# Performance work log

Measured on AMD Instinct MI355X. Metric: run time of the kernel, lower is better.

## Reference

```python
import jax, jax.numpy as jnp
import numpy as np

N_NODES = 50000
N_EDGES = 800000
IN_DIM = 128
OUT_DIM = 64
NEG_SLOPE = 0.01  # torch F.leaky_relu default


def setup_inputs() -> dict:
    key = jax.random.key(0)
    k1, k2, k3, k4, k5 = jax.random.split(key, 5)
    features = jax.random.normal(k1, (N_NODES, IN_DIM), dtype=jnp.float32)
    # xavier-ish scale for weights
    fc_w = jax.random.normal(k2, (OUT_DIM, IN_DIM), dtype=jnp.float32) * (1.0 / np.sqrt(IN_DIM))
    attn_w = jax.random.normal(k3, (2 * OUT_DIM,), dtype=jnp.float32) * (1.0 / np.sqrt(2 * OUT_DIM))
    src = jax.random.randint(k4, (N_EDGES,), 0, N_NODES, dtype=jnp.int32)
    dst = jax.random.randint(k5, (N_EDGES,), 0, N_NODES, dtype=jnp.int32)
    return {"features": features, "fc_w": fc_w, "attn_w": attn_w, "src": src, "dst": dst}


def reference(features, fc_w, attn_w, src, dst):
    n = features.shape[0]
    out_dim = fc_w.shape[0]
    # z = fc(features), [N, out_dim]
    z = features @ fc_w.T
    # attn_fc([z_src || z_dst]) = z_src @ w_src + z_dst @ w_dst
    a_src = z @ attn_w[:out_dim]   # [N]
    a_dst = z @ attn_w[out_dim:]   # [N]
    e = a_src[src] + a_dst[dst]    # [E] per-edge raw score
    e = jnp.where(e > 0, e, NEG_SLOPE * e)  # leaky_relu
    # edge softmax over incoming edges of each dst node
    e_max = jax.ops.segment_max(e, dst, num_segments=n)      # [N]
    w = jnp.exp(e - e_max[dst])                               # [E]
    denom = jax.ops.segment_sum(w, dst, num_segments=n)       # [N]
    # weighted neighbor sum: sum_e alpha_e * z[src_e]
    num = jax.ops.segment_sum(w[:, None] * z[src], dst, num_segments=n)  # [N, out_dim]
    h = num / jnp.where(denom > 0, denom, 1.0)[:, None]
    # activation = elu
    h = jax.nn.elu(h)
    return h
```

## Files before the change

kernel.cpp:

```cpp
#include <hip/hip_runtime.h>
#include <hip/hip_bf16.h>

#define N_NODES 50000
#define N_EDGES 800000
#define IN_DIM 128
#define OUT_DIM 64
#define NEG_SLOPE 0.01f
#define NEG_INF (-3.0e38f)

#define N_STRIPS (N_NODES / 16)
#define Z_BLOCKS ((N_STRIPS + 3) / 4)
#define E_I4 (N_EDGES / 4)

#define NB ((N_NODES + 127) / 128)
#define CAP_B 3072
#define CNT_STRIDE 16
#define EB 100
#define CHUNK_I4 (E_I4 / EB)

typedef __bf16 bf16x8 __attribute__((ext_vector_type(8)));
typedef float f32x4 __attribute__((ext_vector_type(4)));

__device__ __forceinline__ float rlanef(float v, int l) {
  return __uint_as_float(__builtin_amdgcn_readlane(__float_as_uint(v), l));
}
__device__ __forceinline__ int rlanei(int v, int l) {
  return __builtin_amdgcn_readlane(v, l);
}

__device__ __forceinline__ unsigned short f2bf_us(float f) {
  __hip_bfloat16 h = __float2bfloat16(f);
  return *reinterpret_cast<unsigned short*>(&h);
}
__device__ __forceinline__ bf16x8 pack_bf16(float4 lo, float4 hi) {
  union { bf16x8 v; unsigned short u[8]; } r;
  r.u[0] = f2bf_us(lo.x); r.u[1] = f2bf_us(lo.y);
  r.u[2] = f2bf_us(lo.z); r.u[3] = f2bf_us(lo.w);
  r.u[4] = f2bf_us(hi.x); r.u[5] = f2bf_us(hi.y);
  r.u[6] = f2bf_us(hi.z); r.u[7] = f2bf_us(hi.w);
  return r.v;
}

__global__ __launch_bounds__(256) void gat_z_bucket(
    const float* __restrict__ feat, const float* __restrict__ fcw,
    const float* __restrict__ attnw, __hip_bfloat16* __restrict__ z,
    float* __restrict__ asrc, float* __restrict__ adst,
    const int* __restrict__ src, const int* __restrict__ dst,
    int* __restrict__ cnt, unsigned* __restrict__ pairs) {
  if (blockIdx.x >= Z_BLOCKS) {
    __shared__ int hist[NB];
    __shared__ int curs[NB];
    const int tid = threadIdx.x;
    const int i0 = (blockIdx.x - Z_BLOCKS) * CHUNK_I4;
    for (int i = tid; i < NB; i += 256) hist[i] = 0;
    __syncthreads();
    for (int t = i0 + tid; t < i0 + CHUNK_I4; t += 256) {
      int4 d = ((const int4*)dst)[t];
      atomicAdd(&hist[d.x >> 7], 1);
      atomicAdd(&hist[d.y >> 7], 1);
      atomicAdd(&hist[d.z >> 7], 1);
      atomicAdd(&hist[d.w >> 7], 1);
    }
    __syncthreads();
    for (int i = tid; i < NB; i += 256) {
      int h = hist[i];
      curs[i] = h ? atomicAdd(cnt + i * CNT_STRIDE, h) : 0;
    }
    __syncthreads();
    for (int t = i0 + tid; t < i0 + CHUNK_I4; t += 256) {
      int4 s = ((const int4*)src)[t];
      int4 d = ((const int4*)dst)[t];
#define BKT_PUT(dd, ss)                                                    \
  {                                                                        \
    int b = (dd) >> 7;                                                     \
    int r = atomicAdd(&curs[b], 1);                                        \
    if (r < CAP_B)                                                         \
      pairs[(size_t)b * CAP_B + r] =                                       \
          ((unsigned)((dd) & 127) << 16) | (unsigned)(ss);                 \
  }
      BKT_PUT(d.x, s.x)
      BKT_PUT(d.y, s.y)
      BKT_PUT(d.z, s.z)
      BKT_PUT(d.w, s.w)
#undef BKT_PUT
    }
    return;
  }

  const int lane = threadIdx.x & 63;
  const int m = lane & 15;
  const int quad = lane >> 4;
  const int wv = blockIdx.x * 4 + (threadIdx.x >> 6);
  if (wv >= N_STRIPS) return;
  const int n0 = wv * 16;

  bf16x8 bfrag[4][4];
#pragma unroll
  for (int t = 0; t < 4; ++t) {
    const float* wr = fcw + (size_t)(m + 16 * t) * IN_DIM + quad * 8;
#pragma unroll
    for (int c = 0; c < 4; ++c) {
      float4 lo = *(const float4*)(wr + c * 32);
      float4 hi = *(const float4*)(wr + c * 32 + 4);
      bfrag[t][c] = pack_bf16(lo, hi);
    }
  }

  f32x4 acc[4] = {{0.f, 0.f, 0.f, 0.f}, {0.f, 0.f, 0.f, 0.f},
                  {0.f, 0.f, 0.f, 0.f}, {0.f, 0.f, 0.f, 0.f}};
  const float* ar = feat + (size_t)(n0 + m) * IN_DIM + quad * 8;
#pragma unroll
  for (int c = 0; c < 4; ++c) {
    float4 lo = *(const float4*)(ar + c * 32);
    float4 hi = *(const float4*)(ar + c * 32 + 4);
    const bf16x8 af = pack_bf16(lo, hi);
#pragma unroll
    for (int t = 0; t < 4; ++t)
      acc[t] = __builtin_amdgcn_mfma_f32_16x16x32_bf16(af, bfrag[t][c],
                                                       acc[t], 0, 0, 0);
  }

#pragma unroll
  for (int t = 0; t < 4; ++t)
#pragma unroll
    for (int r = 0; r < 4; ++r)
      z[(size_t)(n0 + quad * 4 + r) * OUT_DIM + m + 16 * t] =
          __float2bfloat16(acc[t][r]);

  float aws[4], awd[4];
#pragma unroll
  for (int t = 0; t < 4; ++t) {
    aws[t] = attnw[m + 16 * t];
    awd[t] = attnw[OUT_DIM + m + 16 * t];
  }
  float ps[4], pd[4];
#pragma unroll
  for (int r = 0; r < 4; ++r) {
    float s = 0.f, d = 0.f;
#pragma unroll
    for (int t = 0; t < 4; ++t) {
      s = fmaf(acc[t][r], aws[t], s);
      d = fmaf(acc[t][r], awd[t], d);
    }
    ps[r] = s;
    pd[r] = d;
  }
#pragma unroll
  for (int off = 1; off < 16; off <<= 1) {
#pragma unroll
    for (int r = 0; r < 4; ++r) {
      ps[r] += __shfl_xor(ps[r], off, 64);
      pd[r] += __shfl_xor(pd[r], off, 64);
    }
  }
  if (m == 0) {
#pragma unroll
    for (int r = 0; r < 4; ++r) {
      asrc[n0 + quad * 4 + r] = ps[r];
      adst[n0 + quad * 4 + r] = pd[r];
    }
  }
}

__global__ __launch_bounds__(512) void gat_bucket_scan(
    const int* __restrict__ cnt, int* __restrict__ bbase,
    int* __restrict__ offsets) {
  __shared__ int ps[512];
  const int t = threadIdx.x;
  int tot = (t < NB) ? cnt[t * CNT_STRIDE] : 0;
  ps[t] = tot;
  __syncthreads();
  for (int off = 1; off < 512; off <<= 1) {
    int u = (t >= off) ? ps[t - off] : 0;
    __syncthreads();
    ps[t] += u;
    __syncthreads();
  }
  if (t < NB) bbase[t] = ps[t] - tot;
  if (t == NB - 1) offsets[N_NODES] = ps[t];
}

__global__ __launch_bounds__(256) void gat_build_csr(
    const unsigned* __restrict__ pairs, const int* __restrict__ cnt,
    const int* __restrict__ bbase, int* __restrict__ offsets,
    int* __restrict__ ssorted) {
  __shared__ int hist[128], exo[128], cur[128];
  const int b = blockIdx.x;
  const int tid = threadIdx.x;
  if (tid < 128) hist[tid] = 0;
  __syncthreads();

  const int c = min(cnt[b * CNT_STRIDE], CAP_B);
  const unsigned* bp = pairs + (size_t)b * CAP_B;
  for (int i = tid; i < c; i += 256) atomicAdd(&hist[bp[i] >> 16], 1);
  __syncthreads();

  if (tid < 128) exo[tid] = hist[tid];
  __syncthreads();
  for (int off = 1; off < 128; off <<= 1) {
    int u = (tid >= off && tid < 128) ? exo[tid - off] : 0;
    __syncthreads();
    if (tid < 128) exo[tid] += u;
    __syncthreads();
  }
  const int base = bbase[b];
  if (tid < 128) {
    const int ex = exo[tid] - hist[tid];
    cur[tid] = ex;
    const int node = b * 128 + tid;
    if (node < N_NODES) offsets[node] = base + ex;
  }
  __syncthreads();

  for (int i = tid; i < c; i += 256) {
    const unsigned p = bp[i];
    const int r = atomicAdd(&cur[p >> 16], 1);
    ssorted[base + r] = (int)(p & 0xFFFFu);
  }
}

__global__ __launch_bounds__(256) void gat_agg(
    const __hip_bfloat16* __restrict__ zb, const float* __restrict__ asrc,
    const float* __restrict__ adst, const int* __restrict__ offsets,
    const int* __restrict__ ssorted, float* __restrict__ out) {
  const int lane = threadIdx.x & 63;
  const int cl = lane & 31;
  const int half = lane >> 5;
  const int node = (blockIdx.x * blockDim.x + threadIdx.x) >> 6;
  if (node >= N_NODES) return;
  const unsigned* __restrict__ zp = (const unsigned*)zb;
  const int o0 = offsets[node];
  const int o1 = offsets[node + 1];
  if (o0 == o1) {
    if (half == 0)
      *(float2*)(out + (size_t)node * OUT_DIM + 2 * cl) = make_float2(0.f, 0.f);
    return;
  }
  const float ad = adst[node];

  float m = NEG_INF, dsum = 0.f;
  float2 acc0 = {0.f, 0.f}, acc1 = {0.f, 0.f};
  float2 acc2 = {0.f, 0.f}, acc3 = {0.f, 0.f};

  for (int base = o0; base < o1; base += 64) {
    const int cnt = min(64, o1 - base);
    int s = 0;
    float ev = NEG_INF;
    if (lane < cnt) {
      s = ssorted[base + lane];
      float v = asrc[s] + ad;
      ev = v > 0.f ? v : NEG_SLOPE * v;
    }
    float cm = ev;
#pragma unroll
    for (int off = 32; off; off >>= 1) cm = fmaxf(cm, __shfl_xor(cm, off, 64));
    const float nm = fmaxf(m, cm);
    const float scale = __expf(m - nm);
    dsum *= scale;
    acc0.x *= scale; acc0.y *= scale; acc1.x *= scale; acc1.y *= scale;
    acc2.x *= scale; acc2.y *= scale; acc3.x *= scale; acc3.y *= scale;
    m = nm;

    float w = (lane < cnt) ? __expf(ev - m) : 0.f;
    dsum += w;

    for (int i = 0; i < cnt; i += 8) {
      int sa, sb; float wa, wb;
      sa = rlanei(s, i + 0); sb = rlanei(s, i + 1);
      wa = rlanef(w, i + 0); wb = rlanef(w, i + 1);
      const int s0 = half ? sb : sa; const float w0 = half ? wb : wa;
      sa = rlanei(s, i + 2); sb = rlanei(s, i + 3);
      wa = rlanef(w, i + 2); wb = rlanef(w, i + 3);
      const int s1 = half ? sb : sa; const float w1 = half ? wb : wa;
      sa = rlanei(s, i + 4); sb = rlanei(s, i + 5);
      wa = rlanef(w, i + 4); wb = rlanef(w, i + 5);
      const int s2 = half ? sb : sa; const float w2 = half ? wb : wa;
      sa = rlanei(s, i + 6); sb = rlanei(s, i + 7);
      wa = rlanef(w, i + 6); wb = rlanef(w, i + 7);
      const int s3 = half ? sb : sa; const float w3 = half ? wb : wa;

      const unsigned u0 = zp[(size_t)s0 * 32 + cl];
      const unsigned u1 = zp[(size_t)s1 * 32 + cl];
      const unsigned u2 = zp[(size_t)s2 * 32 + cl];
      const unsigned u3 = zp[(size_t)s3 * 32 + cl];

      acc0.x = fmaf(w0, __uint_as_float(u0 << 16), acc0.x);
      acc0.y = fmaf(w0, __uint_as_float(u0 & 0xffff0000u), acc0.y);
      acc1.x = fmaf(w1, __uint_as_float(u1 << 16), acc1.x);
      acc1.y = fmaf(w1, __uint_as_float(u1 & 0xffff0000u), acc1.y);
      acc2.x = fmaf(w2, __uint_as_float(u2 << 16), acc2.x);
      acc2.y = fmaf(w2, __uint_as_float(u2 & 0xffff0000u), acc2.y);
      acc3.x = fmaf(w3, __uint_as_float(u3 << 16), acc3.x);
      acc3.y = fmaf(w3, __uint_as_float(u3 & 0xffff0000u), acc3.y);
    }
  }
  float ax = (acc0.x + acc1.x) + (acc2.x + acc3.x);
  float ay = (acc0.y + acc1.y) + (acc2.y + acc3.y);
  ax += __shfl_xor(ax, 32, 64);
  ay += __shfl_xor(ay, 32, 64);
#pragma unroll
  for (int off = 32; off; off >>= 1) dsum += __shfl_xor(dsum, off, 64);

  const float inv = 1.f / (dsum > 0.f ? dsum : 1.f);
  float hx = ax * inv, hy = ay * inv;
  hx = hx > 0.f ? hx : expm1f(hx);
  hy = hy > 0.f ? hy : expm1f(hy);
  if (half == 0)
    *(float2*)(out + (size_t)node * OUT_DIM + 2 * cl) = make_float2(hx, hy);
}

extern "C" void kernel_launch(void* const* d_in, const int* in_sizes, int n_in,
                              void* d_out, int out_size, void* d_ws, size_t ws_size,
                              hipStream_t stream) {
  const float* feat  = (const float*)d_in[0];
  const float* fcw   = (const float*)d_in[1];
  const float* attnw = (const float*)d_in[2];
  const int* src     = (const int*)d_in[3];
  const int* dst     = (const int*)d_in[4];
  float* out = (float*)d_out;

  char* ws = (char*)d_ws;
  __hip_bfloat16* z = (__hip_bfloat16*)ws;
  ws += (size_t)N_NODES * OUT_DIM * sizeof(__hip_bfloat16);
  float* asrc = (float*)ws;   ws += (size_t)N_NODES * sizeof(float);
  float* adst = (float*)ws;   ws += (size_t)N_NODES * sizeof(float);
  int* cnt = (int*)ws;        ws += (size_t)NB * CNT_STRIDE * sizeof(int);
  int* bbase = (int*)ws;      ws += (size_t)512 * sizeof(int);
  int* offsets = (int*)ws;    ws += (size_t)(N_NODES + 4) * sizeof(int);
  unsigned* pairs = (unsigned*)ws; ws += (size_t)NB * CAP_B * sizeof(unsigned);
  int* ssorted = (int*)ws;    ws += (size_t)N_EDGES * sizeof(int);

  hipMemsetAsync(cnt, 0, (size_t)NB * CNT_STRIDE * sizeof(int), stream);

  gat_z_bucket<<<Z_BLOCKS + EB, 256, 0, stream>>>(
      feat, fcw, attnw, z, asrc, adst, src, dst, cnt, pairs);
  gat_bucket_scan<<<1, 512, 0, stream>>>(cnt, bbase, offsets);
  gat_build_csr<<<NB, 256, 0, stream>>>(pairs, cnt, bbase, offsets, ssorted);
  gat_agg<<<(N_NODES * 64 + 255) / 256, 256, 0, stream>>>(z, asrc, adst,
                                                          offsets, ssorted, out);
}
```

Before: 147.9 us.

## Fold bucket scan into CSR build and widen aggregation gathers to 16-byte rows

```diff
diff --git a/kernel.cpp b/kernel.cpp
--- a/kernel.cpp
+++ b/kernel.cpp
@@ -1,5 +1,6 @@
 #include <hip/hip_runtime.h>
 #include <hip/hip_bf16.h>
+#include <hip/hip_fp16.h>
 
 #define N_NODES 50000
 #define N_EDGES 800000
@@ -20,13 +21,6 @@
 
 typedef __bf16 bf16x8 __attribute__((ext_vector_type(8)));
 typedef float f32x4 __attribute__((ext_vector_type(4)));
-
-__device__ __forceinline__ float rlanef(float v, int l) {
-  return __uint_as_float(__builtin_amdgcn_readlane(__float_as_uint(v), l));
-}
-__device__ __forceinline__ int rlanei(int v, int l) {
-  return __builtin_amdgcn_readlane(v, l);
-}
 
 __device__ __forceinline__ unsigned short f2bf_us(float f) {
   __hip_bfloat16 h = __float2bfloat16(f);
@@ -39,6 +33,12 @@
   r.u[4] = f2bf_us(hi.x); r.u[5] = f2bf_us(hi.y);
   r.u[6] = f2bf_us(hi.z); r.u[7] = f2bf_us(hi.w);
   return r.v;
+}
+__device__ __forceinline__ float bflo(unsigned u) {
+  return __uint_as_float(u << 16);
+}
+__device__ __forceinline__ float bfhi(unsigned u) {
+  return __uint_as_float(u & 0xffff0000u);
 }
 
 __global__ __launch_bounds__(256) void gat_z_bucket(
@@ -162,33 +162,21 @@
   }
 }
 
-__global__ __launch_bounds__(512) void gat_bucket_scan(
-    const int* __restrict__ cnt, int* __restrict__ bbase,
-    int* __restrict__ offsets) {
-  __shared__ int ps[512];
-  const int t = threadIdx.x;
-  int tot = (t < NB) ? cnt[t * CNT_STRIDE] : 0;
-  ps[t] = tot;
-  __syncthreads();
-  for (int off = 1; off < 512; off <<= 1) {
-    int u = (t >= off) ? ps[t - off] : 0;
-    __syncthreads();
-    ps[t] += u;
-    __syncthreads();
-  }
-  if (t < NB) bbase[t] = ps[t] - tot;
-  if (t == NB - 1) offsets[N_NODES] = ps[t];
-}
-
 __global__ __launch_bounds__(256) void gat_build_csr(
     const unsigned* __restrict__ pairs, const int* __restrict__ cnt,
-    const int* __restrict__ bbase, int* __restrict__ offsets,
-    int* __restrict__ ssorted) {
-  __shared__ int hist[128], exo[128], cur[128];
+    int* __restrict__ offsets, int* __restrict__ ssorted) {
+  __shared__ int hist[128], exo[128], cur[128], wsum[4];
   const int b = blockIdx.x;
   const int tid = threadIdx.x;
+
+  int ls = 0;
+  for (int i = tid; i < b; i += 256) ls += cnt[i * CNT_STRIDE];
+#pragma unroll
+  for (int off = 32; off; off >>= 1) ls += __shfl_xor(ls, off, 64);
+  if ((tid & 63) == 0) wsum[tid >> 6] = ls;
   if (tid < 128) hist[tid] = 0;
   __syncthreads();
+  const int base = wsum[0] + wsum[1] + wsum[2] + wsum[3];
 
   const int c = min(cnt[b * CNT_STRIDE], CAP_B);
   const unsigned* bp = pairs + (size_t)b * CAP_B;
@@ -203,13 +191,13 @@
     if (tid < 128) exo[tid] += u;
     __syncthreads();
   }
-  const int base = bbase[b];
   if (tid < 128) {
     const int ex = exo[tid] - hist[tid];
     cur[tid] = ex;
     const int node = b * 128 + tid;
     if (node < N_NODES) offsets[node] = base + ex;
   }
+  if (b == NB - 1 && tid == 0) offsets[N_NODES] = base + c;
   __syncthreads();
 
   for (int i = tid; i < c; i += 256) {
@@ -224,23 +212,27 @@
     const float* __restrict__ adst, const int* __restrict__ offsets,
     const int* __restrict__ ssorted, float* __restrict__ out) {
   const int lane = threadIdx.x & 63;
-  const int cl = lane & 31;
-  const int half = lane >> 5;
+  const int j = lane & 7;
+  const int eg = lane >> 3;
   const int node = (blockIdx.x * blockDim.x + threadIdx.x) >> 6;
   if (node >= N_NODES) return;
-  const unsigned* __restrict__ zp = (const unsigned*)zb;
+  const uint4* __restrict__ zp4 = (const uint4*)zb;
   const int o0 = offsets[node];
   const int o1 = offsets[node + 1];
+  float4* __restrict__ orow = (float4*)(out + (size_t)node * OUT_DIM);
   if (o0 == o1) {
-    if (half == 0)
-      *(float2*)(out + (size_t)node * OUT_DIM + 2 * cl) = make_float2(0.f, 0.f);
+    if (eg == 0) {
+      const float4 zv = {0.f, 0.f, 0.f, 0.f};
+      orow[2 * j] = zv;
+      orow[2 * j + 1] = zv;
+    }
     return;
   }
   const float ad = adst[node];
 
   float m = NEG_INF, dsum = 0.f;
-  float2 acc0 = {0.f, 0.f}, acc1 = {0.f, 0.f};
-  float2 acc2 = {0.f, 0.f}, acc3 = {0.f, 0.f};
+  float acca[8] = {0.f, 0.f, 0.f, 0.f, 0.f, 0.f, 0.f, 0.f};
+  float accb[8] = {0.f, 0.f, 0.f, 0.f, 0.f, 0.f, 0.f, 0.f};
 
   for (int base = o0; base < o1; base += 64) {
     const int cnt = min(64, o1 - base);
@@ -257,56 +249,76 @@
     const float nm = fmaxf(m, cm);
     const float scale = __expf(m - nm);
     dsum *= scale;
-    acc0.x *= scale; acc0.y *= scale; acc1.x *= scale; acc1.y *= scale;
-    acc2.x *= scale; acc2.y *= scale; acc3.x *= scale; acc3.y *= scale;
+#pragma unroll
+    for (int c = 0; c < 8; ++c) {
+      acca[c] *= scale;
+      accb[c] *= scale;
+    }
     m = nm;
 
-    float w = (lane < cnt) ? __expf(ev - m) : 0.f;
+    const float w = (lane < cnt) ? __expf(ev - m) : 0.f;
     dsum += w;
-
-    for (int i = 0; i < cnt; i += 8) {
-      int sa, sb; float wa, wb;
-      sa = rlanei(s, i + 0); sb = rlanei(s, i + 1);
-      wa = rlanef(w, i + 0); wb = rlanef(w, i + 1);
-      const int s0 = half ? sb : sa; const float w0 = half ? wb : wa;
-      sa = rlanei(s, i + 2); sb = rlanei(s, i + 3);
-      wa = rlanef(w, i + 2); wb = rlanef(w, i + 3);
-      const int s1 = half ? sb : sa; const float w1 = half ? wb : wa;
-      sa = rlanei(s, i + 4); sb = rlanei(s, i + 5);
-      wa = rlanef(w, i + 4); wb = rlanef(w, i + 5);
-      const int s2 = half ? sb : sa; const float w2 = half ? wb : wa;
-      sa = rlanei(s, i + 6); sb = rlanei(s, i + 7);
-      wa = rlanef(w, i + 6); wb = rlanef(w, i + 7);
-      const int s3 = half ? sb : sa; const float w3 = half ? wb : wa;
-
-      const unsigned u0 = zp[(size_t)s0 * 32 + cl];
-      const unsigned u1 = zp[(size_t)s1 * 32 + cl];
-      const unsigned u2 = zp[(size_t)s2 * 32 + cl];
-      const unsigned u3 = zp[(size_t)s3 * 32 + cl];
-
-      acc0.x = fmaf(w0, __uint_as_float(u0 << 16), acc0.x);
-      acc0.y = fmaf(w0, __uint_as_float(u0 & 0xffff0000u), acc0.y);
-      acc1.x = fmaf(w1, __uint_as_float(u1 << 16), acc1.x);
-      acc1.y = fmaf(w1, __uint_as_float(u1 & 0xffff0000u), acc1.y);
-      acc2.x = fmaf(w2, __uint_as_float(u2 << 16), acc2.x);
-      acc2.y = fmaf(w2, __uint_as_float(u2 & 0xffff0000u), acc2.y);
-      acc3.x = fmaf(w3, __uint_as_float(u3 << 16), acc3.x);
-      acc3.y = fmaf(w3, __uint_as_float(u3 & 0xffff0000u), acc3.y);
-    }
-  }
-  float ax = (acc0.x + acc1.x) + (acc2.x + acc3.x);
-  float ay = (acc0.y + acc1.y) + (acc2.y + acc3.y);
-  ax += __shfl_xor(ax, 32, 64);
-  ay += __shfl_xor(ay, 32, 64);
+    const unsigned pk =
+        (unsigned)s |
+        ((unsigned)__half_as_ushort(__float2half(w)) << 16);
+
+    const int ngr = (cnt + 7) >> 3;
+    for (int g = 0; g < ngr; g += 2) {
+      const unsigned pa = __shfl(pk, 8 * g + eg, 64);
+      const int sa = (int)(pa & 0xFFFFu);
+      const float wa = __half2float(__ushort_as_half((unsigned short)(pa >> 16)));
+      const uint4 ua = zp4[(size_t)sa * 8 + j];
+      if (g + 1 < ngr) {
+        const unsigned pb = __shfl(pk, 8 * (g + 1) + eg, 64);
+        const int sb = (int)(pb & 0xFFFFu);
+        const float wb =
+            __half2float(__ushort_as_half((unsigned short)(pb >> 16)));
+        const uint4 ub = zp4[(size_t)sb * 8 + j];
+        accb[0] = fmaf(wb, bflo(ub.x), accb[0]);
+        accb[1] = fmaf(wb, bfhi(ub.x), accb[1]);
+        accb[2] = fmaf(wb, bflo(ub.y), accb[2]);
+        accb[3] = fmaf(wb, bfhi(ub.y), accb[3]);
+        accb[4] = fmaf(wb, bflo(ub.z), accb[4]);
+        accb[5] = fmaf(wb, bfhi(ub.z), accb[5]);
+        accb[6] = fmaf(wb, bflo(ub.w), accb[6]);
+        accb[7] = fmaf(wb, bfhi(ub.w), accb[7]);
+      }
+      acca[0] = fmaf(wa, bflo(ua.x), acca[0]);
+      acca[1] = fmaf(wa, bfhi(ua.x), acca[1]);
+      acca[2] = fmaf(wa, bflo(ua.y), acca[2]);
+      acca[3] = fmaf(wa, bfhi(ua.y), acca[3]);
+      acca[4] = fmaf(wa, bflo(ua.z), acca[4]);
+      acca[5] = fmaf(wa, bfhi(ua.z), acca[5]);
+      acca[6] = fmaf(wa, bflo(ua.w), acca[6]);
+      acca[7] = fmaf(wa, bfhi(ua.w), acca[7]);
+    }
+  }
+
+  float acc[8];
+#pragma unroll
+  for (int c = 0; c < 8; ++c) acc[c] = acca[c] + accb[c];
+#pragma unroll
+  for (int off = 8; off < 64; off <<= 1)
+#pragma unroll
+    for (int c = 0; c < 8; ++c) acc[c] += __shfl_xor(acc[c], off, 64);
 #pragma unroll
   for (int off = 32; off; off >>= 1) dsum += __shfl_xor(dsum, off, 64);
 
-  const float inv = 1.f / (dsum > 0.f ? dsum : 1.f);
-  float hx = ax * inv, hy = ay * inv;
-  hx = hx > 0.f ? hx : expm1f(hx);
-  hy = hy > 0.f ? hy : expm1f(hy);
-  if (half == 0)
-    *(float2*)(out + (size_t)node * OUT_DIM + 2 * cl) = make_float2(hx, hy);
+  if (eg == 0) {
+    const float inv = 1.f / (dsum > 0.f ? dsum : 1.f);
+    float4 r0, r1;
+    float h;
+    h = acc[0] * inv; r0.x = h > 0.f ? h : expm1f(h);
+    h = acc[1] * inv; r0.y = h > 0.f ? h : expm1f(h);
+    h = acc[2] * inv; r0.z = h > 0.f ? h : expm1f(h);
+    h = acc[3] * inv; r0.w = h > 0.f ? h : expm1f(h);
+    h = acc[4] * inv; r1.x = h > 0.f ? h : expm1f(h);
+    h = acc[5] * inv; r1.y = h > 0.f ? h : expm1f(h);
+    h = acc[6] * inv; r1.z = h > 0.f ? h : expm1f(h);
+    h = acc[7] * inv; r1.w = h > 0.f ? h : expm1f(h);
+    orow[2 * j] = r0;
+    orow[2 * j + 1] = r1;
+  }
 }
 
 extern "C" void kernel_launch(void* const* d_in, const int* in_sizes, int n_in,
@@ -325,7 +337,6 @@
   float* asrc = (float*)ws;   ws += (size_t)N_NODES * sizeof(float);
   float* adst = (float*)ws;   ws += (size_t)N_NODES * sizeof(float);
   int* cnt = (int*)ws;        ws += (size_t)NB * CNT_STRIDE * sizeof(int);
-  int* bbase = (int*)ws;      ws += (size_t)512 * sizeof(int);
   int* offsets = (int*)ws;    ws += (size_t)(N_NODES + 4) * sizeof(int);
   unsigned* pairs = (unsigned*)ws; ws += (size_t)NB * CAP_B * sizeof(unsigned);
   int* ssorted = (int*)ws;    ws += (size_t)N_EDGES * sizeof(int);
@@ -334,8 +345,7 @@
 
   gat_z_bucket<<<Z_BLOCKS + EB, 256, 0, stream>>>(
       feat, fcw, attnw, z, asrc, adst, src, dst, cnt, pairs);
-  gat_bucket_scan<<<1, 512, 0, stream>>>(cnt, bbase, offsets);
-  gat_build_csr<<<NB, 256, 0, stream>>>(pairs, cnt, bbase, offsets, ssorted);
+  gat_build_csr<<<NB, 256, 0, stream>>>(pairs, cnt, offsets, ssorted);
   gat_agg<<<(N_NODES * 64 + 255) / 256, 256, 0, stream>>>(z, asrc, adst,
                                                           offsets, ssorted, out);
 }
```

New measurement: 145.8 us. Within noise of the previous version (-1.4%).
